# Kernel tuning notes

Hardware: AMD Instinct MI355X
Metric: run time of the kernel (lower is better)

Reference implementation:

```python
import jax, jax.numpy as jnp
import numpy as np

N, IN_DIM, HEADS, OUT_DIM, EDGE_DIM = 3072, 128, 4, 64, 8
EPS = 1e-5


def setup_inputs() -> dict:
    key = jax.random.key(0)
    ks = jax.random.split(key, 8)
    x = jax.random.normal(ks[0], (N, IN_DIM), dtype=jnp.float32)
    adj = jax.random.randint(ks[1], (N, N), 0, 2, dtype=jnp.int32)
    edge_feats = jax.random.normal(ks[2], (N, N, EDGE_DIM), dtype=jnp.float32)
    W = jax.random.normal(ks[3], (IN_DIM, HEADS * OUT_DIM), dtype=jnp.float32) * (IN_DIM ** -0.5)
    a_src = jax.random.normal(ks[4], (HEADS, OUT_DIM), dtype=jnp.float32) * 0.01
    a_dst = jax.random.normal(ks[5], (HEADS, OUT_DIM), dtype=jnp.float32) * 0.01
    ep_w = jax.random.normal(ks[6], (EDGE_DIM, HEADS), dtype=jnp.float32) * (EDGE_DIM ** -0.5)
    ep_b = jax.random.normal(ks[7], (HEADS,), dtype=jnp.float32) * 0.01
    gamma = jnp.ones((HEADS * OUT_DIM,), dtype=jnp.float32)
    beta = jnp.zeros((HEADS * OUT_DIM,), dtype=jnp.float32)
    return {"x": x, "adj": adj, "edge_feats": edge_feats, "W": W, "a_src": a_src,
            "a_dst": a_dst, "ep_w": ep_w, "ep_b": ep_b, "gamma": gamma, "beta": beta}


def reference(x, adj, edge_feats, W, a_src, a_dst, ep_w, ep_b, gamma, beta):
    n = x.shape[0]
    h = (x @ W).reshape(n, HEADS, OUT_DIM)                      # (N,H,D)
    s_src = jnp.einsum('nhd,hd->nh', h, a_src)                  # (N,H)
    s_dst = jnp.einsum('nhd,hd->nh', h, a_dst)                  # (N,H)
    edge_attn = jnp.einsum('ije,eh->ijh', edge_feats, ep_w) + ep_b  # (N,N,H)
    attn = s_src[:, None, :] + s_dst[None, :, :] + edge_attn    # (N,N,H)
    attn = jax.nn.leaky_relu(attn, 0.2)
    neg = jnp.finfo(attn.dtype).min
    attn = jnp.where((adj == 0)[:, :, None], neg, attn)
    attn = jax.nn.softmax(attn, axis=1)                         # softmax over neighbors j
    # dropout is identity in eval mode
    out = jnp.einsum('ijh,jhd->ihd', attn, h).reshape(n, HEADS * OUT_DIM)
    mean = out.mean(-1, keepdims=True)
    var = out.var(-1, keepdims=True)
    out = (out - mean) * jax.lax.rsqrt(var + EPS) * gamma + beta
    return out
```

## Files before the change

kernel.cpp:

```cpp
#include <hip/hip_runtime.h>
#include <hip/hip_bf16.h>

#define NN     3072
#define INDIM  128
#define NH     4
#define DD     64
#define CC     256
#define EE     8
#define NODE_T 8
#define TI     4
#define BJ     128
#define NT     (NN / BJ)
#define PTJ    136

typedef short short8v __attribute__((ext_vector_type(8)));
typedef unsigned short ushort8v __attribute__((ext_vector_type(8)));
typedef float float4v __attribute__((ext_vector_type(4)));

__device__ __forceinline__ float bf2f(unsigned short u) {
    return __uint_as_float(((unsigned int)u) << 16);
}
__device__ __forceinline__ unsigned short f2bf(float f) {
    unsigned int u = __float_as_uint(f);
    u += 0x7fffu + ((u >> 16) & 1u);
    return (unsigned short)(u >> 16);
}

__global__ __launch_bounds__(256) void hproj(
    const float* __restrict__ x,
    const float* __restrict__ W,
    const float* __restrict__ a_src,
    const float* __restrict__ a_dst,
    unsigned short* __restrict__ ht,
    float* __restrict__ s_src,
    float* __restrict__ s_dst)
{
    const int tid = threadIdx.x;
    const int n0  = blockIdx.x * NODE_T;
    const int h   = tid >> 6, lane = tid & 63;

    float acc[NODE_T] = {};
#pragma unroll 4
    for (int k = 0; k < INDIM; ++k) {
        const float wv = W[(size_t)k * CC + tid];
#pragma unroll
        for (int n = 0; n < NODE_T; ++n)
            acc[n] = fmaf(x[(size_t)(n0 + n) * INDIM + k], wv, acc[n]);
    }

    ushort8v hv;
#pragma unroll
    for (int n = 0; n < NODE_T; ++n) hv[n] = f2bf(acc[n]);
    *reinterpret_cast<ushort8v*>(ht + (size_t)tid * NN + n0) = hv;

    const float asv = a_src[h * DD + lane];
    const float adv = a_dst[h * DD + lane];
#pragma unroll
    for (int n = 0; n < NODE_T; ++n) {
        float s1 = acc[n] * asv, s2 = acc[n] * adv;
#pragma unroll
        for (int off = 32; off > 0; off >>= 1) {
            s1 += __shfl_xor(s1, off, 64);
            s2 += __shfl_xor(s2, off, 64);
        }
        if (lane == 0) {
            s_src[(size_t)(n0 + n) * NH + h] = s1;
            s_dst[(size_t)(n0 + n) * NH + h] = s2;
        }
    }
}

__global__ __launch_bounds__(256) void gat_fused(
    const int* __restrict__ adj,
    const float* __restrict__ ef,
    const unsigned short* __restrict__ ht,
    const float* __restrict__ s_src,
    const float* __restrict__ s_dst,
    const float* __restrict__ ep_w,
    const float* __restrict__ ep_b,
    const float* __restrict__ gamma,
    const float* __restrict__ beta,
    float* __restrict__ out)
{
    __shared__ unsigned short pt[2][NH][16][PTJ];
    __shared__ float ll[TI][NH];
    __shared__ float ln[TI][CC];

    const int tid  = threadIdx.x;
    const int w    = tid >> 6;
    const int lane = tid & 63;
    const int l15  = lane & 15;
    const int q    = lane >> 4;
    const int i0   = blockIdx.x * TI;

    {
        unsigned int* p4 = reinterpret_cast<unsigned int*>(&pt[0][0][0][0]);
        const int ndw = 2 * NH * 16 * PTJ / 2;
        for (int t = tid; t < ndw; t += 256) p4[t] = 0u;
    }

    float epw[EE][NH], epb[NH];
#pragma unroll
    for (int e = 0; e < EE; ++e)
#pragma unroll
        for (int h = 0; h < NH; ++h) epw[e][h] = ep_w[e * NH + h];
#pragma unroll
    for (int h = 0; h < NH; ++h) epb[h] = ep_b[h];
    const float4 ssrc4 = *reinterpret_cast<const float4*>(s_src + (size_t)(i0 + w) * NH);
    const float ssrc[NH] = {ssrc4.x, ssrc4.y, ssrc4.z, ssrc4.w};

    const unsigned short* Bbase = ht + (size_t)(w * DD + l15) * NN;
    const size_t ef_row  = ((size_t)(i0 + w) * NN) * EE;
    const size_t adj_row = (size_t)(i0 + w) * NN;

    float4v accf[4];
#pragma unroll
    for (int f = 0; f < 4; ++f) accf[f] = (float4v){0.f, 0.f, 0.f, 0.f};
    float l_loc[NH] = {0.f, 0.f, 0.f, 0.f};

    __syncthreads();

    {
        const int j2 = 2 * lane;
        const int2  a2  = *reinterpret_cast<const int2*>(adj + adj_row + j2);
        const float4 e0a = *reinterpret_cast<const float4*>(ef + ef_row + (size_t)j2 * EE);
        const float4 e1a = *reinterpret_cast<const float4*>(ef + ef_row + (size_t)j2 * EE + 4);
        const float4 e0b = *reinterpret_cast<const float4*>(ef + ef_row + (size_t)j2 * EE + 8);
        const float4 e1b = *reinterpret_cast<const float4*>(ef + ef_row + (size_t)j2 * EE + 12);
        const float4 sda = *reinterpret_cast<const float4*>(s_dst + (size_t)j2 * NH);
        const float4 sdb = *reinterpret_cast<const float4*>(s_dst + (size_t)(j2 + 1) * NH);
        const float eva[EE] = {e0a.x, e0a.y, e0a.z, e0a.w, e1a.x, e1a.y, e1a.z, e1a.w};
        const float evb[EE] = {e0b.x, e0b.y, e0b.z, e0b.w, e1b.x, e1b.y, e1b.z, e1b.w};
        const float sdha[NH] = {sda.x, sda.y, sda.z, sda.w};
        const float sdhb[NH] = {sdb.x, sdb.y, sdb.z, sdb.w};
#pragma unroll
        for (int h = 0; h < NH; ++h) {
            float sa = ssrc[h] + sdha[h] + epb[h];
            float sb = ssrc[h] + sdhb[h] + epb[h];
#pragma unroll
            for (int e = 0; e < EE; ++e) {
                sa = fmaf(eva[e], epw[e][h], sa);
                sb = fmaf(evb[e], epw[e][h], sb);
            }
            sa = (sa > 0.f) ? sa : 0.2f * sa;
            sb = (sb > 0.f) ? sb : 0.2f * sb;
            const float pa = (a2.x == 0) ? 0.f : __expf(sa);
            const float pb = (a2.y == 0) ? 0.f : __expf(sb);
            const unsigned int ba = f2bf(pa), bb = f2bf(pb);
            l_loc[h] += bf2f((unsigned short)ba) + bf2f((unsigned short)bb);
            reinterpret_cast<unsigned int*>(&pt[0][h][w][0])[lane] = ba | (bb << 16);
        }
    }
    __syncthreads();

    int buf = 0;
    for (int t = 0; t < NT; ++t) {
        int2  a2_n = {0, 0};
        float4 e0a_n, e1a_n, e0b_n, e1b_n, sda_n, sdb_n;
        if (t + 1 < NT) {
            const int j2 = (t + 1) * BJ + 2 * lane;
            a2_n  = *reinterpret_cast<const int2*>(adj + adj_row + j2);
            e0a_n = *reinterpret_cast<const float4*>(ef + ef_row + (size_t)j2 * EE);
            e1a_n = *reinterpret_cast<const float4*>(ef + ef_row + (size_t)j2 * EE + 4);
            e0b_n = *reinterpret_cast<const float4*>(ef + ef_row + (size_t)j2 * EE + 8);
            e1b_n = *reinterpret_cast<const float4*>(ef + ef_row + (size_t)j2 * EE + 12);
            sda_n = *reinterpret_cast<const float4*>(s_dst + (size_t)j2 * NH);
            sdb_n = *reinterpret_cast<const float4*>(s_dst + (size_t)(j2 + 1) * NH);
        }

#pragma unroll
        for (int ks = 0; ks < 4; ++ks) {
            const short8v a = *reinterpret_cast<const short8v*>(&pt[buf][w][l15][ks * 32 + q * 8]);
            const size_t jb = (size_t)(t * BJ + ks * 32 + q * 8);
#pragma unroll
            for (int f = 0; f < 4; ++f) {
                const short8v b = *reinterpret_cast<const short8v*>(Bbase + (size_t)(f * 16) * NN + jb);
                accf[f] = __builtin_amdgcn_mfma_f32_16x16x32_bf16(a, b, accf[f], 0, 0, 0);
            }
        }

        if (t + 1 < NT) {
            const float eva[EE] = {e0a_n.x, e0a_n.y, e0a_n.z, e0a_n.w, e1a_n.x, e1a_n.y, e1a_n.z, e1a_n.w};
            const float evb[EE] = {e0b_n.x, e0b_n.y, e0b_n.z, e0b_n.w, e1b_n.x, e1b_n.y, e1b_n.z, e1b_n.w};
            const float sdha[NH] = {sda_n.x, sda_n.y, sda_n.z, sda_n.w};
            const float sdhb[NH] = {sdb_n.x, sdb_n.y, sdb_n.z, sdb_n.w};
#pragma unroll
            for (int h = 0; h < NH; ++h) {
                float sa = ssrc[h] + sdha[h] + epb[h];
                float sb = ssrc[h] + sdhb[h] + epb[h];
#pragma unroll
                for (int e = 0; e < EE; ++e) {
                    sa = fmaf(eva[e], epw[e][h], sa);
                    sb = fmaf(evb[e], epw[e][h], sb);
                }
                sa = (sa > 0.f) ? sa : 0.2f * sa;
                sb = (sb > 0.f) ? sb : 0.2f * sb;
                const float pa = (a2_n.x == 0) ? 0.f : __expf(sa);
                const float pb = (a2_n.y == 0) ? 0.f : __expf(sb);
                const unsigned int ba = f2bf(pa), bb = f2bf(pb);
                l_loc[h] += bf2f((unsigned short)ba) + bf2f((unsigned short)bb);
                reinterpret_cast<unsigned int*>(&pt[buf ^ 1][h][w][0])[lane] = ba | (bb << 16);
            }
        }
        __syncthreads();
        buf ^= 1;
    }

#pragma unroll
    for (int h = 0; h < NH; ++h) {
        float v = l_loc[h];
#pragma unroll
        for (int off = 32; off > 0; off >>= 1) v += __shfl_xor(v, off, 64);
        if (lane == 0) ll[w][h] = v;
    }
    __syncthreads();

    if (q == 0) {
        float rinv[TI];
#pragma unroll
        for (int r = 0; r < TI; ++r) rinv[r] = 1.f / ll[r][w];
#pragma unroll
        for (int f = 0; f < 4; ++f)
#pragma unroll
            for (int r = 0; r < TI; ++r)
                ln[r][w * DD + f * 16 + l15] = accf[f][r] * rinv[r];
    }
    __syncthreads();

    {
        const float v0 = ln[w][lane],       v1 = ln[w][64 + lane];
        const float v2 = ln[w][128 + lane], v3 = ln[w][192 + lane];
        float s1 = v0 + v1 + v2 + v3;
        float s2 = v0 * v0 + v1 * v1 + v2 * v2 + v3 * v3;
#pragma unroll
        for (int off = 32; off > 0; off >>= 1) {
            s1 += __shfl_xor(s1, off, 64);
            s2 += __shfl_xor(s2, off, 64);
        }
        const float mean = s1 * (1.f / CC);
        const float var  = s2 * (1.f / CC) - mean * mean;
        const float rstd = rsqrtf(var + 1e-5f);
        float* op = out + (size_t)(i0 + w) * CC;
        op[lane]       = (v0 - mean) * rstd * gamma[lane]       + beta[lane];
        op[64 + lane]  = (v1 - mean) * rstd * gamma[64 + lane]  + beta[64 + lane];
        op[128 + lane] = (v2 - mean) * rstd * gamma[128 + lane] + beta[128 + lane];
        op[192 + lane] = (v3 - mean) * rstd * gamma[192 + lane] + beta[192 + lane];
    }
}

extern "C" void kernel_launch(void* const* d_in, const int* in_sizes, int n_in,
                              void* d_out, int out_size, void* d_ws, size_t ws_size,
                              hipStream_t stream) {
    const float* x     = (const float*)d_in[0];
    const int*   adj   = (const int*)d_in[1];
    const float* ef    = (const float*)d_in[2];
    const float* W     = (const float*)d_in[3];
    const float* a_src = (const float*)d_in[4];
    const float* a_dst = (const float*)d_in[5];
    const float* ep_w  = (const float*)d_in[6];
    const float* ep_b  = (const float*)d_in[7];
    const float* gamma = (const float*)d_in[8];
    const float* beta  = (const float*)d_in[9];

    float* s_src = (float*)d_ws;
    float* s_dst = s_src + (size_t)NN * NH;
    unsigned short* ht = (unsigned short*)(s_dst + (size_t)NN * NH);

    hipLaunchKernelGGL(hproj, dim3(NN / NODE_T), dim3(256), 0, stream,
                       x, W, a_src, a_dst, ht, s_src, s_dst);
    hipLaunchKernelGGL(gat_fused, dim3(NN / TI), dim3(256), 0, stream,
                       adj, ef, ht, s_src, s_dst, ep_w, ep_b, gamma, beta,
                       (float*)d_out);
}
```

Baseline: 562.8 us.

## Use 16-row MFMA tiles with split-J partials and separate LayerNorm kernel

Each attention block now handles 16 destination rows instead of 4, so every B fragment of h feeds a full 16-row MFMA tile rather than one padded with zero rows, cutting redundant h reads per row. The j dimension is split four ways across blocks, and partial numerators and denominators go to workspace. A new kernel sums the partials and applies softmax normalisation and LayerNorm. h is stored in a fragment-swizzled layout so each lane's B load is contiguous. Register loads are explicitly scheduled ahead of the MFMAs. The cost is extra workspace traffic of about 12 MB of partials and a third kernel launch.

```diff
diff --git a/kernel.cpp b/kernel.cpp
--- a/kernel.cpp
+++ b/kernel.cpp
@@ -1,5 +1,4 @@
 #include <hip/hip_runtime.h>
-#include <hip/hip_bf16.h>
 
 #define NN     3072
 #define INDIM  128
@@ -8,10 +7,13 @@
 #define CC     256
 #define EE     8
 #define NODE_T 8
-#define TI     4
-#define BJ     128
-#define NT     (NN / BJ)
-#define PTJ    136
+#define TI16   16
+#define BJ     64
+#define JSPLIT 4
+#define JRANGE (NN / JSPLIT)
+#define NTS    (JRANGE / BJ)
+#define PTJ    72
+#define NCH    (NN / 32)
 
 typedef short short8v __attribute__((ext_vector_type(8)));
 typedef unsigned short ushort8v __attribute__((ext_vector_type(8)));
@@ -24,6 +26,9 @@
     unsigned int u = __float_as_uint(f);
     u += 0x7fffu + ((u >> 16) & 1u);
     return (unsigned short)(u >> 16);
+}
+__device__ __forceinline__ float rfl(float f) {
+    return __int_as_float(__builtin_amdgcn_readfirstlane(__float_as_int(f)));
 }
 
 __global__ __launch_bounds__(256) void hproj(
@@ -31,7 +36,7 @@
     const float* __restrict__ W,
     const float* __restrict__ a_src,
     const float* __restrict__ a_dst,
-    unsigned short* __restrict__ ht,
+    unsigned short* __restrict__ htf,
     float* __restrict__ s_src,
     float* __restrict__ s_dst)
 {
@@ -51,7 +56,10 @@
     ushort8v hv;
 #pragma unroll
     for (int n = 0; n < NODE_T; ++n) hv[n] = f2bf(acc[n]);
-    *reinterpret_cast<ushort8v*>(ht + (size_t)tid * NN + n0) = hv;
+    unsigned short* dst = htf
+        + (size_t)((h * 4 + (lane >> 4)) * NCH + (n0 >> 5)) * 512
+        + (size_t)((((n0 >> 3) & 3) * 16 + (lane & 15)) * 8);
+    *reinterpret_cast<ushort8v*>(dst) = hv;
 
     const float asv = a_src[h * DD + lane];
     const float adv = a_dst[h * DD + lane];
@@ -70,181 +78,177 @@
     }
 }
 
-__global__ __launch_bounds__(256) void gat_fused(
+__global__ __launch_bounds__(256, 3) void gat_fused(
     const int* __restrict__ adj,
     const float* __restrict__ ef,
-    const unsigned short* __restrict__ ht,
+    const unsigned short* __restrict__ htf,
     const float* __restrict__ s_src,
     const float* __restrict__ s_dst,
     const float* __restrict__ ep_w,
     const float* __restrict__ ep_b,
+    float* __restrict__ out_part,
+    float* __restrict__ l_part)
+{
+    __shared__ unsigned short pt[2][NH][16][PTJ];
+
+    const int tid  = threadIdx.x;
+    const int rw   = tid >> 6;
+    const int lane = tid & 63;
+    const int l15  = lane & 15;
+    const int q    = lane >> 4;
+    const int bid  = blockIdx.x;
+    const int s    = bid & (JSPLIT - 1);
+    const int i0   = (bid >> 2) * TI16;
+    const int jb0  = s * JRANGE;
+
+    float epw[EE][NH], epb4[NH];
+#pragma unroll
+    for (int e = 0; e < EE; ++e)
+#pragma unroll
+        for (int h = 0; h < NH; ++h) epw[e][h] = ep_w[e * NH + h];
+#pragma unroll
+    for (int h = 0; h < NH; ++h) epb4[h] = ep_b[h];
+    float ssrc[4][4];
+#pragma unroll
+    for (int r = 0; r < 4; ++r)
+#pragma unroll
+        for (int h = 0; h < NH; ++h)
+            ssrc[r][h] = rfl(s_src[(size_t)(i0 + rw * 4 + r) * NH + h]);
+
+    float4v acc[4];
+#pragma unroll
+    for (int f = 0; f < 4; ++f) acc[f] = (float4v){0.f, 0.f, 0.f, 0.f};
+    float l_loc[4][4] = {};
+
+    float4 efA[4], efB[4], sd4;
+    int    ajr[4];
+
+#define LOADP(JN) {                                                          \
+        const int jj = (JN) + lane;                                          \
+        sd4 = *reinterpret_cast<const float4*>(s_dst + (size_t)jj * NH);     \
+        _Pragma("unroll")                                                    \
+        for (int r = 0; r < 4; ++r) {                                        \
+            const size_t ro = (size_t)(i0 + rw * 4 + r) * NN;                \
+            ajr[r] = adj[ro + jj];                                           \
+            const float* ep = ef + (ro + jj) * EE;                           \
+            efA[r] = *reinterpret_cast<const float4*>(ep);                   \
+            efB[r] = *reinterpret_cast<const float4*>(ep + 4);               \
+        } }
+
+#define SCOREP(NB) {                                                         \
+        const float sdh[4] = {sd4.x, sd4.y, sd4.z, sd4.w};                   \
+        _Pragma("unroll")                                                    \
+        for (int r = 0; r < 4; ++r) {                                        \
+            const float ev[EE] = {efA[r].x, efA[r].y, efA[r].z, efA[r].w,    \
+                                  efB[r].x, efB[r].y, efB[r].z, efB[r].w};   \
+            _Pragma("unroll")                                                \
+            for (int h = 0; h < NH; ++h) {                                   \
+                float sc = ssrc[r][h] + sdh[h] + epb4[h];                    \
+                _Pragma("unroll")                                            \
+                for (int e = 0; e < EE; ++e)                                 \
+                    sc = fmaf(ev[e], epw[e][h], sc);                         \
+                sc = (sc > 0.f) ? sc : 0.2f * sc;                            \
+                const float p = (ajr[r] == 0) ? 0.f : __expf(sc);            \
+                const unsigned short bb = f2bf(p);                           \
+                l_loc[r][h] += bf2f(bb);                                     \
+                pt[NB][h][rw * 4 + r][lane] = bb;                            \
+            } } }
+
+    LOADP(jb0);
+    SCOREP(0);
+    __syncthreads();
+
+    int buf = 0;
+    for (int t = 0; t < NTS; ++t) {
+        const int jb   = jb0 + t * BJ;
+        const int cid0 = jb >> 5;
+        const bool pf  = (t + 1 < NTS);
+
+        short8v bfrag[2][4];
+#pragma unroll
+        for (int ks = 0; ks < 2; ++ks)
+#pragma unroll
+            for (int f = 0; f < 4; ++f)
+                bfrag[ks][f] = *reinterpret_cast<const short8v*>(
+                    htf + (size_t)((rw * 4 + f) * NCH + cid0 + ks) * 512 + lane * 8);
+        __builtin_amdgcn_sched_barrier(0);
+
+        if (pf) LOADP(jb + BJ);
+        __builtin_amdgcn_sched_barrier(0);
+
+#pragma unroll
+        for (int ks = 0; ks < 2; ++ks) {
+            const short8v a = *reinterpret_cast<const short8v*>(
+                &pt[buf][rw][l15][ks * 32 + q * 8]);
+#pragma unroll
+            for (int f = 0; f < 4; ++f)
+                acc[f] = __builtin_amdgcn_mfma_f32_16x16x32_bf16(a, bfrag[ks][f], acc[f], 0, 0, 0);
+        }
+
+        if (pf) SCOREP(buf ^ 1);
+        __syncthreads();
+        buf ^= 1;
+    }
+
+#pragma unroll
+    for (int r = 0; r < 4; ++r)
+#pragma unroll
+        for (int h = 0; h < NH; ++h) {
+            float v = l_loc[r][h];
+#pragma unroll
+            for (int off = 32; off > 0; off >>= 1) v += __shfl_xor(v, off, 64);
+            if (lane == 0)
+                l_part[((size_t)s * NN + i0 + rw * 4 + r) * NH + h] = v;
+        }
+
+#pragma unroll
+    for (int f = 0; f < 4; ++f)
+#pragma unroll
+        for (int rg = 0; rg < 4; ++rg)
+            out_part[((size_t)s * NN + i0 + q * 4 + rg) * CC + rw * DD + f * 16 + l15] = acc[f][rg];
+#undef LOADP
+#undef SCOREP
+}
+
+__global__ __launch_bounds__(256) void gat_ln(
+    const float* __restrict__ out_part,
+    const float* __restrict__ l_part,
     const float* __restrict__ gamma,
     const float* __restrict__ beta,
     float* __restrict__ out)
 {
-    __shared__ unsigned short pt[2][NH][16][PTJ];
-    __shared__ float ll[TI][NH];
-    __shared__ float ln[TI][CC];
-
-    const int tid  = threadIdx.x;
-    const int w    = tid >> 6;
-    const int lane = tid & 63;
-    const int l15  = lane & 15;
-    const int q    = lane >> 4;
-    const int i0   = blockIdx.x * TI;
-
-    {
-        unsigned int* p4 = reinterpret_cast<unsigned int*>(&pt[0][0][0][0]);
-        const int ndw = 2 * NH * 16 * PTJ / 2;
-        for (int t = tid; t < ndw; t += 256) p4[t] = 0u;
-    }
-
-    float epw[EE][NH], epb[NH];
-#pragma unroll
-    for (int e = 0; e < EE; ++e)
-#pragma unroll
-        for (int h = 0; h < NH; ++h) epw[e][h] = ep_w[e * NH + h];
-#pragma unroll
-    for (int h = 0; h < NH; ++h) epb[h] = ep_b[h];
-    const float4 ssrc4 = *reinterpret_cast<const float4*>(s_src + (size_t)(i0 + w) * NH);
-    const float ssrc[NH] = {ssrc4.x, ssrc4.y, ssrc4.z, ssrc4.w};
-
-    const unsigned short* Bbase = ht + (size_t)(w * DD + l15) * NN;
-    const size_t ef_row  = ((size_t)(i0 + w) * NN) * EE;
-    const size_t adj_row = (size_t)(i0 + w) * NN;
-
-    float4v accf[4];
-#pragma unroll
-    for (int f = 0; f < 4; ++f) accf[f] = (float4v){0.f, 0.f, 0.f, 0.f};
-    float l_loc[NH] = {0.f, 0.f, 0.f, 0.f};
-
-    __syncthreads();
-
-    {
-        const int j2 = 2 * lane;
-        const int2  a2  = *reinterpret_cast<const int2*>(adj + adj_row + j2);
-        const float4 e0a = *reinterpret_cast<const float4*>(ef + ef_row + (size_t)j2 * EE);
-        const float4 e1a = *reinterpret_cast<const float4*>(ef + ef_row + (size_t)j2 * EE + 4);
-        const float4 e0b = *reinterpret_cast<const float4*>(ef + ef_row + (size_t)j2 * EE + 8);
-        const float4 e1b = *reinterpret_cast<const float4*>(ef + ef_row + (size_t)j2 * EE + 12);
-        const float4 sda = *reinterpret_cast<const float4*>(s_dst + (size_t)j2 * NH);
-        const float4 sdb = *reinterpret_cast<const float4*>(s_dst + (size_t)(j2 + 1) * NH);
-        const float eva[EE] = {e0a.x, e0a.y, e0a.z, e0a.w, e1a.x, e1a.y, e1a.z, e1a.w};
-        const float evb[EE] = {e0b.x, e0b.y, e0b.z, e0b.w, e1b.x, e1b.y, e1b.z, e1b.w};
-        const float sdha[NH] = {sda.x, sda.y, sda.z, sda.w};
-        const float sdhb[NH] = {sdb.x, sdb.y, sdb.z, sdb.w};
-#pragma unroll
-        for (int h = 0; h < NH; ++h) {
-            float sa = ssrc[h] + sdha[h] + epb[h];
-            float sb = ssrc[h] + sdhb[h] + epb[h];
-#pragma unroll
-            for (int e = 0; e < EE; ++e) {
-                sa = fmaf(eva[e], epw[e][h], sa);
-                sb = fmaf(evb[e], epw[e][h], sb);
-            }
-            sa = (sa > 0.f) ? sa : 0.2f * sa;
-            sb = (sb > 0.f) ? sb : 0.2f * sb;
-            const float pa = (a2.x == 0) ? 0.f : __expf(sa);
-            const float pb = (a2.y == 0) ? 0.f : __expf(sb);
-            const unsigned int ba = f2bf(pa), bb = f2bf(pb);
-            l_loc[h] += bf2f((unsigned short)ba) + bf2f((unsigned short)bb);
-            reinterpret_cast<unsigned int*>(&pt[0][h][w][0])[lane] = ba | (bb << 16);
-        }
-    }
-    __syncthreads();
-
-    int buf = 0;
-    for (int t = 0; t < NT; ++t) {
-        int2  a2_n = {0, 0};
-        float4 e0a_n, e1a_n, e0b_n, e1b_n, sda_n, sdb_n;
-        if (t + 1 < NT) {
-            const int j2 = (t + 1) * BJ + 2 * lane;
-            a2_n  = *reinterpret_cast<const int2*>(adj + adj_row + j2);
-            e0a_n = *reinterpret_cast<const float4*>(ef + ef_row + (size_t)j2 * EE);
-            e1a_n = *reinterpret_cast<const float4*>(ef + ef_row + (size_t)j2 * EE + 4);
-            e0b_n = *reinterpret_cast<const float4*>(ef + ef_row + (size_t)j2 * EE + 8);
-            e1b_n = *reinterpret_cast<const float4*>(ef + ef_row + (size_t)j2 * EE + 12);
-            sda_n = *reinterpret_cast<const float4*>(s_dst + (size_t)j2 * NH);
-            sdb_n = *reinterpret_cast<const float4*>(s_dst + (size_t)(j2 + 1) * NH);
-        }
-
-#pragma unroll
-        for (int ks = 0; ks < 4; ++ks) {
-            const short8v a = *reinterpret_cast<const short8v*>(&pt[buf][w][l15][ks * 32 + q * 8]);
-            const size_t jb = (size_t)(t * BJ + ks * 32 + q * 8);
-#pragma unroll
-            for (int f = 0; f < 4; ++f) {
-                const short8v b = *reinterpret_cast<const short8v*>(Bbase + (size_t)(f * 16) * NN + jb);
-                accf[f] = __builtin_amdgcn_mfma_f32_16x16x32_bf16(a, b, accf[f], 0, 0, 0);
-            }
-        }
-
-        if (t + 1 < NT) {
-            const float eva[EE] = {e0a_n.x, e0a_n.y, e0a_n.z, e0a_n.w, e1a_n.x, e1a_n.y, e1a_n.z, e1a_n.w};
-            const float evb[EE] = {e0b_n.x, e0b_n.y, e0b_n.z, e0b_n.w, e1b_n.x, e1b_n.y, e1b_n.z, e1b_n.w};
-            const float sdha[NH] = {sda_n.x, sda_n.y, sda_n.z, sda_n.w};
-            const float sdhb[NH] = {sdb_n.x, sdb_n.y, sdb_n.z, sdb_n.w};
-#pragma unroll
-            for (int h = 0; h < NH; ++h) {
-                float sa = ssrc[h] + sdha[h] + epb[h];
-                float sb = ssrc[h] + sdhb[h] + epb[h];
-#pragma unroll
-                for (int e = 0; e < EE; ++e) {
-                    sa = fmaf(eva[e], epw[e][h], sa);
-                    sb = fmaf(evb[e], epw[e][h], sb);
-                }
-                sa = (sa > 0.f) ? sa : 0.2f * sa;
-                sb = (sb > 0.f) ? sb : 0.2f * sb;
-                const float pa = (a2_n.x == 0) ? 0.f : __expf(sa);
-                const float pb = (a2_n.y == 0) ? 0.f : __expf(sb);
-                const unsigned int ba = f2bf(pa), bb = f2bf(pb);
-                l_loc[h] += bf2f((unsigned short)ba) + bf2f((unsigned short)bb);
-                reinterpret_cast<unsigned int*>(&pt[buf ^ 1][h][w][0])[lane] = ba | (bb << 16);
-            }
-        }
-        __syncthreads();
-        buf ^= 1;
-    }
-
-#pragma unroll
-    for (int h = 0; h < NH; ++h) {
-        float v = l_loc[h];
-#pragma unroll
-        for (int off = 32; off > 0; off >>= 1) v += __shfl_xor(v, off, 64);
-        if (lane == 0) ll[w][h] = v;
-    }
-    __syncthreads();
-
-    if (q == 0) {
-        float rinv[TI];
-#pragma unroll
-        for (int r = 0; r < TI; ++r) rinv[r] = 1.f / ll[r][w];
-#pragma unroll
-        for (int f = 0; f < 4; ++f)
-#pragma unroll
-            for (int r = 0; r < TI; ++r)
-                ln[r][w * DD + f * 16 + l15] = accf[f][r] * rinv[r];
-    }
-    __syncthreads();
-
-    {
-        const float v0 = ln[w][lane],       v1 = ln[w][64 + lane];
-        const float v2 = ln[w][128 + lane], v3 = ln[w][192 + lane];
-        float s1 = v0 + v1 + v2 + v3;
-        float s2 = v0 * v0 + v1 * v1 + v2 * v2 + v3 * v3;
-#pragma unroll
-        for (int off = 32; off > 0; off >>= 1) {
-            s1 += __shfl_xor(s1, off, 64);
-            s2 += __shfl_xor(s2, off, 64);
-        }
-        const float mean = s1 * (1.f / CC);
-        const float var  = s2 * (1.f / CC) - mean * mean;
-        const float rstd = rsqrtf(var + 1e-5f);
-        float* op = out + (size_t)(i0 + w) * CC;
-        op[lane]       = (v0 - mean) * rstd * gamma[lane]       + beta[lane];
-        op[64 + lane]  = (v1 - mean) * rstd * gamma[64 + lane]  + beta[64 + lane];
-        op[128 + lane] = (v2 - mean) * rstd * gamma[128 + lane] + beta[128 + lane];
-        op[192 + lane] = (v3 - mean) * rstd * gamma[192 + lane] + beta[192 + lane];
+    const int tid = threadIdx.x, w = tid >> 6, lane = tid & 63;
+    const int i = blockIdx.x * 4 + w;
+
+    float v[4];
+#pragma unroll
+    for (int k = 0; k < 4; ++k) {
+        float a = 0.f;
+#pragma unroll
+        for (int sp = 0; sp < JSPLIT; ++sp)
+            a += out_part[((size_t)sp * NN + i) * CC + k * 64 + lane];
+        float lb = 0.f;
+#pragma unroll
+        for (int sp = 0; sp < JSPLIT; ++sp)
+            lb += l_part[((size_t)sp * NN + i) * NH + k];
+        v[k] = a / lb;
+    }
+
+    float s1 = v[0] + v[1] + v[2] + v[3];
+    float s2 = v[0] * v[0] + v[1] * v[1] + v[2] * v[2] + v[3] * v[3];
+#pragma unroll
+    for (int off = 32; off > 0; off >>= 1) {
+        s1 += __shfl_xor(s1, off, 64);
+        s2 += __shfl_xor(s2, off, 64);
+    }
+    const float mean = s1 * (1.f / CC);
+    const float var  = s2 * (1.f / CC) - mean * mean;
+    const float rstd = rsqrtf(var + 1e-5f);
+    float* op = out + (size_t)i * CC;
+#pragma unroll
+    for (int k = 0; k < 4; ++k) {
+        const int c = k * 64 + lane;
+        op[c] = (v[k] - mean) * rstd * gamma[c] + beta[c];
     }
 }
 
@@ -264,11 +268,15 @@
 
     float* s_src = (float*)d_ws;
     float* s_dst = s_src + (size_t)NN * NH;
-    unsigned short* ht = (unsigned short*)(s_dst + (size_t)NN * NH);
+    unsigned short* htf = (unsigned short*)(s_dst + (size_t)NN * NH);
+    float* out_part = (float*)(htf + (size_t)NN * CC);
+    float* l_part   = out_part + (size_t)JSPLIT * NN * CC;
+    (void)ws_size; (void)in_sizes; (void)n_in; (void)out_size;
 
     hipLaunchKernelGGL(hproj, dim3(NN / NODE_T), dim3(256), 0, stream,
-                       x, W, a_src, a_dst, ht, s_src, s_dst);
-    hipLaunchKernelGGL(gat_fused, dim3(NN / TI), dim3(256), 0, stream,
-                       adj, ef, ht, s_src, s_dst, ep_w, ep_b, gamma, beta,
-                       (float*)d_out);
-}
+                       x, W, a_src, a_dst, htf, s_src, s_dst);
+    hipLaunchKernelGGL(gat_fused, dim3((NN / TI16) * JSPLIT), dim3(256), 0, stream,
+                       adj, ef, htf, s_src, s_dst, ep_w, ep_b, out_part, l_part);
+    hipLaunchKernelGGL(gat_ln, dim3(NN / 4), dim3(256), 0, stream,
+                       out_part, l_part, gamma, beta, (float*)d_out);
+}
```

Result: faster. 472.1 us (-16.1%).
